# Performance work log

Measured on AMD Instinct MI355X. Metric: run time of the kernel, lower is better.

The kernel has to match this reference:

```python
import jax, jax.numpy as jnp
import numpy as np

S, LC = 4096, 16
N_WORD, N_CHAR = 100000, 128
CHAR_DIM, CHAR_HIDDEN = 64, 128
N_DIM, N_HIDDEN, N_TAG = 256, 512, 64


def setup_inputs() -> dict:
    key = jax.random.key(0)
    ks = jax.random.split(key, 16)
    rn = lambda k, shape, s=0.1: (jax.random.normal(k, shape, jnp.float32) * s)
    inp = {
        'char_emb': rn(ks[0], (N_CHAR, CHAR_DIM), 1.0),
        'char_Wih': rn(ks[1], (4 * CHAR_HIDDEN, CHAR_DIM)),
        'char_Whh': rn(ks[2], (4 * CHAR_HIDDEN, CHAR_HIDDEN)),
        'char_bih': rn(ks[3], (4 * CHAR_HIDDEN,)),
        'char_bhh': rn(ks[4], (4 * CHAR_HIDDEN,)),
        'word_emb': rn(ks[5], (N_WORD, N_DIM), 1.0),
        'Wih': rn(ks[6], (4 * N_HIDDEN, N_DIM + CHAR_HIDDEN)),
        'Whh': rn(ks[7], (4 * N_HIDDEN, N_HIDDEN)),
        'bih': rn(ks[8], (4 * N_HIDDEN,)),
        'bhh': rn(ks[9], (4 * N_HIDDEN,)),
        'W1': rn(ks[10], (N_TAG, N_HIDDEN)),
        'b1': rn(ks[11], (N_TAG,)),
        'x': jax.random.randint(ks[12], (S,), 0, N_WORD),
        'chars': jax.random.randint(ks[13], (S, LC), 0, N_CHAR),
        'char_lens': jax.random.randint(ks[14], (S,), 1, LC + 1),
    }
    return inp


def _lstm(xs, mask, Wih, Whh, bih, bhh):
    # xs: [T, B, In], mask: [T, B] bool. PyTorch gate order: i, f, g, o.
    T, B, _ = xs.shape
    H = Whh.shape[1]
    def step(carry, inp):
        h, c = carry
        x_t, m_t = inp
        g = x_t @ Wih.T + bih + h @ Whh.T + bhh  # [B, 4H]
        i, f, gg, o = jnp.split(g, 4, axis=-1)
        c_new = jax.nn.sigmoid(f) * c + jax.nn.sigmoid(i) * jnp.tanh(gg)
        h_new = jax.nn.sigmoid(o) * jnp.tanh(c_new)
        m = m_t[:, None]
        h2 = jnp.where(m, h_new, h)
        c2 = jnp.where(m, c_new, c)
        return (h2, c2), h2
    init = (jnp.zeros((B, H), xs.dtype), jnp.zeros((B, H), xs.dtype))
    (h_fin, _), hs = jax.lax.scan(step, init, (xs, mask))
    return hs, h_fin


def reference(char_emb, char_Wih, char_Whh, char_bih, char_bhh,
              word_emb, Wih, Whh, bih, bhh, W1, b1,
              x, chars, char_lens):
    # --- char-level LSTM, all S words batched (replaces per-word Python loop) ---
    cx = char_emb[chars]                      # [S, LC, char_dim]
    cx = jnp.transpose(cx, (1, 0, 2))         # [LC, S, char_dim]
    cmask = jnp.arange(LC)[:, None] < char_lens[None, :]  # [LC, S]
    _, char_h = _lstm(cx, cmask, char_Wih, char_Whh, char_bih, char_bhh)  # [S, char_hidden]

    # --- word-level LSTM over the sentence (batch 1, as in original) ---
    wx = word_emb[x]                          # [S, n_dim]
    feat = jnp.concatenate([wx, char_h], axis=-1)[:, None, :]  # [S, 1, n_dim+char_hidden]
    wmask = jnp.ones((feat.shape[0], 1), bool)
    hs, _ = _lstm(feat, wmask, Wih, Whh, bih, bhh)  # [S, 1, n_hidden]
    hs = hs[:, 0, :]

    logits = hs @ W1.T + b1                   # [S, n_tag]
    return jax.nn.log_softmax(logits, axis=-1)
```

## Files before the change

### kernel.cpp

```cpp
#include <hip/hip_runtime.h>
#include <hip/hip_bf16.h>


#define OFF_FLAG  0
#define OFF_CEMB  16
#define OFF_CWIH  8208
#define OFF_CBIH  40976
#define OFF_CBHH  41488
#define OFF_CWHH  42000
#define OFF_BIH   107536
#define OFF_BHH   109584
#define OFF_W1T   111632
#define OFF_CGE   144400
#define OFF_CH    209936
#define OFF_XP2   734224
#define OFF_HH    4928528

#define SENT 0xFFFFFFFFu

__device__ __forceinline__ float sigf(float x) { return 1.0f / (1.0f + __expf(-x)); }
__device__ __forceinline__ float tanh_f(float x) { return 2.0f * sigf(2.0f * x) - 1.0f; }
__device__ __forceinline__ float b2f_lo(unsigned u) { return __uint_as_float(u << 16); }
__device__ __forceinline__ float b2f_hi(unsigned u) { return __uint_as_float(u & 0xFFFF0000u); }
__device__ __forceinline__ float4 dec2(uint2 u) {
    return make_float4(b2f_lo(u.x), b2f_hi(u.x), b2f_lo(u.y), b2f_hi(u.y));
}

__global__ void detect_kernel(const unsigned* __restrict__ w, int* __restrict__ flagp) {
    unsigned v = w[threadIdx.x];
    unsigned e = (v >> 7) & 0xFF;
    int inr = (e >= 100 && e <= 140) ? 1 : 0;
    unsigned long long m = __ballot(inr);
    if (threadIdx.x == 0) flagp[0] = (__popcll(m) >= 56) ? 1 : 0;
}

__global__ void convf_kernel(const void* __restrict__ s, float* __restrict__ d,
                             int n, const int* __restrict__ flagp) {
    int i = blockIdx.x * 256 + threadIdx.x;
    if (i >= n) return;
    d[i] = flagp[0] ? __bfloat162float(((const __hip_bfloat16*)s)[i])
                    : ((const float*)s)[i];
}

__global__ void w1t_kernel(const void* __restrict__ W1, float* __restrict__ W1T,
                           const int* __restrict__ flagp) {
    int i = blockIdx.x * 256 + threadIdx.x;
    int j = i & 63, k = i >> 6;
    W1T[i] = flagp[0] ? __bfloat162float(((const __hip_bfloat16*)W1)[j * 512 + k])
                      : ((const float*)W1)[j * 512 + k];
}

__global__ void __launch_bounds__(256) cge_kernel(
    const float* __restrict__ cemb, const float* __restrict__ cWih,
    const float* __restrict__ cbih, const float* __restrict__ cbhh,
    float* __restrict__ cge)
{
    __shared__ float xe[64];
    int c = blockIdx.x, tid = threadIdx.x;
    if (tid < 64) xe[tid] = cemb[c * 64 + tid];
    __syncthreads();
#pragma unroll
    for (int rep = 0; rep < 2; ++rep) {
        int j = rep * 256 + tid;
        float acc = cbih[j] + cbhh[j];
#pragma unroll 8
        for (int k = 0; k < 64; ++k)
            acc += xe[k] * cWih[j * 64 + k];
        cge[c * 512 + j] = acc;
    }
}

__global__ void __launch_bounds__(256) char_lstm_kernel(
    const float* __restrict__ cge, const float* __restrict__ Whh,
    const int* __restrict__ chars, const int* __restrict__ lens,
    float* __restrict__ char_h)
{
    __shared__ float hls[16][128];
    int tid = threadIdx.x;
    int wl = tid >> 4, sl = tid & 15;
    int w = blockIdx.x * 16 + wl;
    int len = lens[w];
    const int* cw = chars + w * 16;
    float c[8];
#pragma unroll
    for (int q = 0; q < 8; ++q) { c[q] = 0.0f; hls[wl][sl * 8 + q] = 0.0f; }

    for (int t = 0; t < 16; ++t) {
        __syncthreads();
        int ch = cw[t];
        const float* xg = cge + ch * 512;
        float acc[4][8];
#pragma unroll
        for (int g = 0; g < 4; ++g)
#pragma unroll
            for (int q = 0; q < 8; ++q)
                acc[g][q] = xg[g * 128 + sl * 8 + q];

        const float4* h4 = (const float4*)hls[wl];
#pragma unroll
        for (int g = 0; g < 4; ++g) {
            const float4* wbase = ((const float4*)Whh) + (g * 128 + sl * 8) * 32;
            for (int k4 = 0; k4 < 32; ++k4) {
                float4 hv = h4[k4];
#pragma unroll
                for (int q = 0; q < 8; ++q) {
                    float4 wv = wbase[q * 32 + k4];
                    acc[g][q] += wv.x * hv.x + wv.y * hv.y + wv.z * hv.z + wv.w * hv.w;
                }
            }
        }
        __syncthreads();
        if (t < len) {
#pragma unroll
            for (int q = 0; q < 8; ++q) {
                float iv = sigf(acc[0][q]);
                float fv = sigf(acc[1][q]);
                float gv = tanh_f(acc[2][q]);
                float ov = sigf(acc[3][q]);
                c[q] = fv * c[q] + iv * gv;
                hls[wl][sl * 8 + q] = ov * tanh_f(c[q]);
            }
        }
    }
    __syncthreads();
#pragma unroll
    for (int q = 0; q < 8; ++q)
        char_h[w * 128 + sl * 8 + q] = hls[wl][sl * 8 + q];
}

__global__ void __launch_bounds__(256) xp2_kernel(
    const void* __restrict__ wemb, const int* __restrict__ x,
    const float* __restrict__ char_h, const void* __restrict__ Wraw,
    const float* __restrict__ bih, const float* __restrict__ bhh,
    __hip_bfloat16* __restrict__ xp2, const int* __restrict__ flagp)
{
    __shared__ float feat[16][384];
    int flag = flagp[0];
    int tid = threadIdx.x, tl = tid >> 4, sl = tid & 15;
    int t = blockIdx.x * 16 + tl;
    int xw = x[t];
    for (int idx = sl; idx < 384; idx += 16) {
        float v;
        if (idx < 256)
            v = flag ? __bfloat162float(((const __hip_bfloat16*)wemb)[(size_t)xw * 256 + idx])
                     : ((const float*)wemb)[(size_t)xw * 256 + idx];
        else
            v = char_h[t * 128 + (idx - 256)];
        feat[tl][idx] = v;
    }
    __syncthreads();

    const float4* f4 = (const float4*)feat[tl];
    for (int rb = 0; rb < 4; ++rb) {
        int r0 = rb * 512 + sl * 32;
        for (int qc = 0; qc < 4; ++qc) {
            int rr = r0 + qc * 8;
            float acc[8];
#pragma unroll
            for (int q = 0; q < 8; ++q)
                acc[q] = bih[rr + q] + bhh[rr + q];
            if (!flag) {
                const float4* wb = ((const float4*)Wraw) + (size_t)rr * 96;
                for (int k4 = 0; k4 < 96; ++k4) {
                    float4 fv = f4[k4];
#pragma unroll
                    for (int q = 0; q < 8; ++q) {
                        float4 wv = wb[q * 96 + k4];
                        acc[q] += wv.x * fv.x + wv.y * fv.y + wv.z * fv.z + wv.w * fv.w;
                    }
                }
            } else {
                const uint2* wb = ((const uint2*)Wraw) + (size_t)rr * 96;
                for (int k4 = 0; k4 < 96; ++k4) {
                    float4 fv = f4[k4];
#pragma unroll
                    for (int q = 0; q < 8; ++q) {
                        uint2 wv = wb[q * 96 + k4];
                        acc[q] += b2f_lo(wv.x) * fv.x + b2f_hi(wv.x) * fv.y
                                + b2f_lo(wv.y) * fv.z + b2f_hi(wv.y) * fv.w;
                    }
                }
            }
#pragma unroll
            for (int q = 0; q < 8; ++q)
                xp2[(size_t)t * 2048 + rr + q] = __float2bfloat16(acc[q]);
        }
    }
}

__global__ void __launch_bounds__(256, 1) word_lstm_kernel(
    const __hip_bfloat16* __restrict__ xp2, const void* __restrict__ Whh_raw,
    float* __restrict__ h_hist, const int* __restrict__ flagp)
{
    __shared__ float hbuf[4][576];
    int flag = flagp[0];
    int tid = threadIdx.x;
    int wave = tid >> 6, lane = tid & 63;
    int wgid = blockIdx.x * 4 + wave;
    int sp = lane >> 5;
    int g  = (lane >> 3) & 3;
    int kk = lane & 7;
    int slot = wgid * 2 + sp;
    int grow = g * 512 + slot;

    float4 w00, w01, w02, w03, w04, w05, w06, w07;
    float4 w08, w09, w10, w11, w12, w13, w14, w15;
    if (!flag) {
        const float4* wr = (const float4*)((const float*)Whh_raw + (size_t)grow * 512 + kk * 64);
        w00 = wr[0];  w01 = wr[1];  w02 = wr[2];  w03 = wr[3];
        w04 = wr[4];  w05 = wr[5];  w06 = wr[6];  w07 = wr[7];
        w08 = wr[8];  w09 = wr[9];  w10 = wr[10]; w11 = wr[11];
        w12 = wr[12]; w13 = wr[13]; w14 = wr[14]; w15 = wr[15];
    } else {
        const uint2* wr = (const uint2*)((const unsigned short*)Whh_raw + (size_t)grow * 512 + kk * 64);
        w00 = dec2(wr[0]);  w01 = dec2(wr[1]);  w02 = dec2(wr[2]);  w03 = dec2(wr[3]);
        w04 = dec2(wr[4]);  w05 = dec2(wr[5]);  w06 = dec2(wr[6]);  w07 = dec2(wr[7]);
        w08 = dec2(wr[8]);  w09 = dec2(wr[9]);  w10 = dec2(wr[10]); w11 = dec2(wr[11]);
        w12 = dec2(wr[12]); w13 = dec2(wr[13]); w14 = dec2(wr[14]); w15 = dec2(wr[15]);
    }

    unsigned* hview = (unsigned*)h_hist;
    const unsigned short* xpr = (const unsigned short*)xp2;
    float* wbuf = hbuf[wave];
    float c = 0.0f;
    int dead = 0;

    unsigned short xraw = xpr[grow];

    for (int t = 0; t < 4096; ++t) {
        unsigned short xraw_nx = (t < 4095) ? xpr[(size_t)(t + 1) * 2048 + grow] : (unsigned short)0;

        if (t == 0) {
#pragma unroll
            for (int i = 0; i < 8; ++i)
                wbuf[(2 * i + (lane >> 5)) * 36 + (lane & 31)] = 0.0f;
        } else {
            const unsigned* src = hview + (size_t)(t - 1) * 512 + lane;
            unsigned v[8];
            unsigned spins = 0;
            for (;;) {
#pragma unroll
                for (int i = 0; i < 8; ++i)
                    v[i] = __hip_atomic_load(src + (size_t)i * 64, __ATOMIC_RELAXED,
                                             __HIP_MEMORY_SCOPE_AGENT);
                int ok = 1;
#pragma unroll
                for (int i = 0; i < 8; ++i) ok &= (v[i] != SENT);
                if (dead || __all(ok)) break;
                if (++spins > (1u << 22)) { dead = 1; break; }
            }
            if (dead) {
#pragma unroll
                for (int i = 0; i < 8; ++i)
                    if (v[i] == SENT) v[i] = __float_as_uint(12345.0f);
            }
#pragma unroll
            for (int i = 0; i < 8; ++i)
                wbuf[(2 * i + (lane >> 5)) * 36 + (lane & 31)] = __uint_as_float(v[i]);
        }

        const float4* p0 = (const float4*)(wbuf + kk * 72);
        const float4* p1 = (const float4*)(wbuf + kk * 72 + 36);
        float a0 = 0.0f, a1 = 0.0f, a2 = 0.0f, a3 = 0.0f;
        {
            float4 hv;
#define FMA4_(A, W, HV) A += (W).x*(HV).x + (W).y*(HV).y + (W).z*(HV).z + (W).w*(HV).w
            hv = p0[0]; FMA4_(a0, w00, hv);  hv = p0[1]; FMA4_(a1, w01, hv);
            hv = p0[2]; FMA4_(a2, w02, hv);  hv = p0[3]; FMA4_(a3, w03, hv);
            hv = p0[4]; FMA4_(a0, w04, hv);  hv = p0[5]; FMA4_(a1, w05, hv);
            hv = p0[6]; FMA4_(a2, w06, hv);  hv = p0[7]; FMA4_(a3, w07, hv);
            hv = p1[0]; FMA4_(a0, w08, hv);  hv = p1[1]; FMA4_(a1, w09, hv);
            hv = p1[2]; FMA4_(a2, w10, hv);  hv = p1[3]; FMA4_(a3, w11, hv);
            hv = p1[4]; FMA4_(a0, w12, hv);  hv = p1[5]; FMA4_(a1, w13, hv);
            hv = p1[6]; FMA4_(a2, w14, hv);  hv = p1[7]; FMA4_(a3, w15, hv);
#undef FMA4_
        }
        float acc = (a0 + a1) + (a2 + a3);
        acc += __shfl_xor(acc, 1);
        acc += __shfl_xor(acc, 2);
        acc += __shfl_xor(acc, 4);
        float gvt = acc + __bfloat162float(*(const __hip_bfloat16*)&xraw);

        float iv = __shfl(gvt, sp * 32 + 0);
        float fv = __shfl(gvt, sp * 32 + 8);
        float gg = __shfl(gvt, sp * 32 + 16);
        float ov = __shfl(gvt, sp * 32 + 24);
        c = sigf(fv) * c + sigf(iv) * tanh_f(gg);
        float h = sigf(ov) * tanh_f(c);

        if ((lane & 31) == 0)
            __hip_atomic_store(hview + (size_t)t * 512 + slot,
                               __float_as_uint(h),
                               __ATOMIC_RELAXED, __HIP_MEMORY_SCOPE_AGENT);

        xraw = xraw_nx;
    }
}

__global__ void __launch_bounds__(64) out_kernel(
    const float* __restrict__ h_hist, const float* __restrict__ W1T,
    const void* __restrict__ b1raw, void* __restrict__ out,
    const int* __restrict__ flagp)
{
    __shared__ float hb[512];
    int flag = flagp[0];
    int t = blockIdx.x, j = threadIdx.x;
    const float4* src = (const float4*)(h_hist + (size_t)t * 512);
    ((float4*)hb)[j * 2] = src[j * 2];
    ((float4*)hb)[j * 2 + 1] = src[j * 2 + 1];
    __syncthreads();

    float acc = flag ? __bfloat162float(((const __hip_bfloat16*)b1raw)[j])
                     : ((const float*)b1raw)[j];
#pragma unroll 8
    for (int k = 0; k < 512; ++k)
        acc += hb[k] * W1T[k * 64 + j];

    float m = acc;
#pragma unroll
    for (int o = 32; o; o >>= 1) m = fmaxf(m, __shfl_xor(m, o));
    float e = __expf(acc - m);
    float s = e;
#pragma unroll
    for (int o = 32; o; o >>= 1) s += __shfl_xor(s, o);
    float r = acc - m - __logf(s);
    if (flag) ((__hip_bfloat16*)out)[t * 64 + j] = __float2bfloat16(r);
    else      ((float*)out)[t * 64 + j] = r;
}

extern "C" void kernel_launch(void* const* d_in, const int* in_sizes, int n_in,
                              void* d_out, int out_size, void* d_ws, size_t ws_size,
                              hipStream_t stream)
{
    (void)in_sizes; (void)n_in; (void)out_size; (void)ws_size;
    const void* char_emb = d_in[0];
    const void* char_Wih = d_in[1];
    const void* char_Whh = d_in[2];
    const void* char_bih = d_in[3];
    const void* char_bhh = d_in[4];
    const void* word_emb = d_in[5];
    const void* Wih      = d_in[6];
    const void* Whh      = d_in[7];
    const void* bih      = d_in[8];
    const void* bhh      = d_in[9];
    const void* W1       = d_in[10];
    const void* b1       = d_in[11];
    const int* x     = (const int*)d_in[12];
    const int* chars = (const int*)d_in[13];
    const int* lens  = (const int*)d_in[14];

    float* ws    = (float*)d_ws;
    int*   flagp = (int*)(ws + OFF_FLAG);
    float* cembf = ws + OFF_CEMB;
    float* cWihf = ws + OFF_CWIH;
    float* cbihf = ws + OFF_CBIH;
    float* cbhhf = ws + OFF_CBHH;
    float* cWhhf = ws + OFF_CWHH;
    float* bihf  = ws + OFF_BIH;
    float* bhhf  = ws + OFF_BHH;
    float* W1T   = ws + OFF_W1T;
    float* cge   = ws + OFF_CGE;
    float* charh = ws + OFF_CH;
    __hip_bfloat16* xp2 = (__hip_bfloat16*)(ws + OFF_XP2);
    float* hh    = ws + OFF_HH;

    hipMemsetAsync(hh, 0xFF, (size_t)4096 * 512 * 4, stream);

    detect_kernel<<<1, 64, 0, stream>>>((const unsigned*)char_emb, flagp);

    convf_kernel<<<(8192 + 255) / 256, 256, 0, stream>>>(char_emb, cembf, 8192, flagp);
    convf_kernel<<<(32768 + 255) / 256, 256, 0, stream>>>(char_Wih, cWihf, 32768, flagp);
    convf_kernel<<<2, 256, 0, stream>>>(char_bih, cbihf, 512, flagp);
    convf_kernel<<<2, 256, 0, stream>>>(char_bhh, cbhhf, 512, flagp);
    convf_kernel<<<(65536 + 255) / 256, 256, 0, stream>>>(char_Whh, cWhhf, 65536, flagp);
    convf_kernel<<<8, 256, 0, stream>>>(bih, bihf, 2048, flagp);
    convf_kernel<<<8, 256, 0, stream>>>(bhh, bhhf, 2048, flagp);
    w1t_kernel<<<128, 256, 0, stream>>>(W1, W1T, flagp);

    cge_kernel<<<128, 256, 0, stream>>>(cembf, cWihf, cbihf, cbhhf, cge);
    char_lstm_kernel<<<256, 256, 0, stream>>>(cge, cWhhf, chars, lens, charh);
    xp2_kernel<<<256, 256, 0, stream>>>(word_emb, x, charh, Wih, bihf, bhhf, xp2, flagp);
    word_lstm_kernel<<<64, 256, 0, stream>>>(xp2, Whh, hh, flagp);
    out_kernel<<<4096, 64, 0, stream>>>(hh, W1T, b1, d_out, flagp);
}
```

Baseline: 14.65 ms.

## Pack word-LSTM hidden exchange into bf16 pairs with 16 large workgroups

The word-level LSTM moves from 64 blocks of 256 threads to 16 blocks of 1024 threads. Each block gathers its 32 hidden outputs in shared memory behind a barrier and publishes them as packed bf16 pairs with one store per lane. Each block reads its own slice from shared memory at full precision and polls only the other blocks' words. This halves the bytes moved through global memory per step and cuts the number of polling producers, at the cost of a __syncthreads per step and bf16 rounding of the exchanged hidden state. The output kernel is updated to read bf16 hidden history.

```diff
diff --git a/kernel.cpp b/kernel.cpp
--- a/kernel.cpp
+++ b/kernel.cpp
@@ -25,6 +25,11 @@
 __device__ __forceinline__ float4 dec2(uint2 u) {
     return make_float4(b2f_lo(u.x), b2f_hi(u.x), b2f_lo(u.y), b2f_hi(u.y));
 }
+__device__ __forceinline__ unsigned f2bf_bits(float f) {
+    unsigned b = __float_as_uint(f);
+    b += 0x7FFFu + ((b >> 16) & 1u);
+    return b >> 16;
+}
 
 __global__ void detect_kernel(const unsigned* __restrict__ w, int* __restrict__ flagp) {
     unsigned v = w[threadIdx.x];
@@ -188,20 +193,22 @@
     }
 }
 
-__global__ void __launch_bounds__(256, 1) word_lstm_kernel(
+__global__ void __launch_bounds__(1024, 4) word_lstm_kernel(
     const __hip_bfloat16* __restrict__ xp2, const void* __restrict__ Whh_raw,
-    float* __restrict__ h_hist, const int* __restrict__ flagp)
-{
-    __shared__ float hbuf[4][576];
+    unsigned* __restrict__ hview, const int* __restrict__ flagp)
+{
+    __shared__ float hbuf[16][576];
+    __shared__ float hout[2][32];
     int flag = flagp[0];
+    int wg = blockIdx.x;
     int tid = threadIdx.x;
     int wave = tid >> 6, lane = tid & 63;
-    int wgid = blockIdx.x * 4 + wave;
     int sp = lane >> 5;
     int g  = (lane >> 3) & 3;
     int kk = lane & 7;
-    int slot = wgid * 2 + sp;
+    int slot = wg * 32 + wave * 2 + sp;
     int grow = g * 512 + slot;
+    int ownidx = ((lane >> 4) == (wg & 3)) ? (wg >> 2) : -1;
 
     float4 w00, w01, w02, w03, w04, w05, w06, w07;
     float4 w08, w09, w10, w11, w12, w13, w14, w15;
@@ -218,45 +225,60 @@
         w08 = dec2(wr[8]);  w09 = dec2(wr[9]);  w10 = dec2(wr[10]); w11 = dec2(wr[11]);
         w12 = dec2(wr[12]); w13 = dec2(wr[13]); w14 = dec2(wr[14]); w15 = dec2(wr[15]);
     }
-
-    unsigned* hview = (unsigned*)h_hist;
+#define PIN4(a,b,c,d) asm volatile("" : "+v"(a.x),"+v"(a.y),"+v"(a.z),"+v"(a.w), \
+    "+v"(b.x),"+v"(b.y),"+v"(b.z),"+v"(b.w), "+v"(c.x),"+v"(c.y),"+v"(c.z),"+v"(c.w), \
+    "+v"(d.x),"+v"(d.y),"+v"(d.z),"+v"(d.w))
+    PIN4(w00, w01, w02, w03); PIN4(w04, w05, w06, w07);
+    PIN4(w08, w09, w10, w11); PIN4(w12, w13, w14, w15);
+#undef PIN4
+
     const unsigned short* xpr = (const unsigned short*)xp2;
     float* wbuf = hbuf[wave];
     float c = 0.0f;
     int dead = 0;
 
-    unsigned short xraw = xpr[grow];
-
     for (int t = 0; t < 4096; ++t) {
-        unsigned short xraw_nx = (t < 4095) ? xpr[(size_t)(t + 1) * 2048 + grow] : (unsigned short)0;
+        unsigned short xraw = xpr[(size_t)t * 2048 + grow];
 
         if (t == 0) {
 #pragma unroll
             for (int i = 0; i < 8; ++i)
                 wbuf[(2 * i + (lane >> 5)) * 36 + (lane & 31)] = 0.0f;
         } else {
-            const unsigned* src = hview + (size_t)(t - 1) * 512 + lane;
-            unsigned v[8];
+            const unsigned* src = hview + (size_t)(t - 1) * 256;
+            const float* houtprev = hout[(t - 1) & 1];
+            unsigned v[4];
             unsigned spins = 0;
             for (;;) {
 #pragma unroll
-                for (int i = 0; i < 8; ++i)
-                    v[i] = __hip_atomic_load(src + (size_t)i * 64, __ATOMIC_RELAXED,
+                for (int i = 0; i < 4; ++i)
+                    v[i] = __hip_atomic_load(src + lane + i * 64, __ATOMIC_RELAXED,
                                              __HIP_MEMORY_SCOPE_AGENT);
                 int ok = 1;
 #pragma unroll
-                for (int i = 0; i < 8; ++i) ok &= (v[i] != SENT);
+                for (int i = 0; i < 4; ++i) ok &= (i == ownidx) | (v[i] != SENT);
                 if (dead || __all(ok)) break;
                 if (++spins > (1u << 22)) { dead = 1; break; }
             }
             if (dead) {
 #pragma unroll
-                for (int i = 0; i < 8; ++i)
-                    if (v[i] == SENT) v[i] = __float_as_uint(12345.0f);
-            }
-#pragma unroll
-            for (int i = 0; i < 8; ++i)
-                wbuf[(2 * i + (lane >> 5)) * 36 + (lane & 31)] = __uint_as_float(v[i]);
+                for (int i = 0; i < 4; ++i)
+                    if (i != ownidx && v[i] == SENT) v[i] = 0x3f803f80u;
+            }
+#pragma unroll
+            for (int i = 0; i < 4; ++i) {
+                int ch = (lane >> 4) + 4 * i;
+                float f0, f1;
+                if (i == ownidx) {
+                    f0 = houtprev[2 * (lane & 15)];
+                    f1 = houtprev[2 * (lane & 15) + 1];
+                } else {
+                    f0 = b2f_lo(v[i]);
+                    f1 = b2f_hi(v[i]);
+                }
+                wbuf[ch * 36 + 2 * (lane & 15)]     = f0;
+                wbuf[ch * 36 + 2 * (lane & 15) + 1] = f1;
+            }
         }
 
         const float4* p0 = (const float4*)(wbuf + kk * 72);
@@ -288,26 +310,34 @@
         c = sigf(fv) * c + sigf(iv) * tanh_f(gg);
         float h = sigf(ov) * tanh_f(c);
 
-        if ((lane & 31) == 0)
-            __hip_atomic_store(hview + (size_t)t * 512 + slot,
-                               __float_as_uint(h),
+        if ((lane & 31) == 0) hout[t & 1][wave * 2 + sp] = h;
+        __syncthreads();
+
+        if (wave == 0 && lane < 16) {
+            unsigned u0 = f2bf_bits(hout[t & 1][2 * lane]);
+            unsigned u1 = f2bf_bits(hout[t & 1][2 * lane + 1]);
+            __hip_atomic_store(hview + (size_t)t * 256 + wg * 16 + lane,
+                               u0 | (u1 << 16),
                                __ATOMIC_RELAXED, __HIP_MEMORY_SCOPE_AGENT);
-
-        xraw = xraw_nx;
+        }
     }
 }
 
 __global__ void __launch_bounds__(64) out_kernel(
-    const float* __restrict__ h_hist, const float* __restrict__ W1T,
+    const unsigned short* __restrict__ hh16, const float* __restrict__ W1T,
     const void* __restrict__ b1raw, void* __restrict__ out,
     const int* __restrict__ flagp)
 {
     __shared__ float hb[512];
     int flag = flagp[0];
     int t = blockIdx.x, j = threadIdx.x;
-    const float4* src = (const float4*)(h_hist + (size_t)t * 512);
-    ((float4*)hb)[j * 2] = src[j * 2];
-    ((float4*)hb)[j * 2 + 1] = src[j * 2 + 1];
+    const unsigned* src = (const unsigned*)(hh16 + (size_t)t * 512);
+#pragma unroll
+    for (int kq = 0; kq < 4; ++kq) {
+        unsigned u = src[j * 4 + kq];
+        hb[j * 8 + 2 * kq]     = b2f_lo(u);
+        hb[j * 8 + 2 * kq + 1] = b2f_hi(u);
+    }
     __syncthreads();
 
     float acc = flag ? __bfloat162float(((const __hip_bfloat16*)b1raw)[j])
@@ -362,9 +392,9 @@
     float* cge   = ws + OFF_CGE;
     float* charh = ws + OFF_CH;
     __hip_bfloat16* xp2 = (__hip_bfloat16*)(ws + OFF_XP2);
-    float* hh    = ws + OFF_HH;
-
-    hipMemsetAsync(hh, 0xFF, (size_t)4096 * 512 * 4, stream);
+    unsigned short* hh16 = (unsigned short*)(ws + OFF_HH);
+
+    hipMemsetAsync(hh16, 0xFF, (size_t)4096 * 512 * 2, stream);
 
     detect_kernel<<<1, 64, 0, stream>>>((const unsigned*)char_emb, flagp);
 
@@ -380,6 +410,6 @@
     cge_kernel<<<128, 256, 0, stream>>>(cembf, cWihf, cbihf, cbhhf, cge);
     char_lstm_kernel<<<256, 256, 0, stream>>>(cge, cWhhf, chars, lens, charh);
     xp2_kernel<<<256, 256, 0, stream>>>(word_emb, x, charh, Wih, bihf, bhhf, xp2, flagp);
-    word_lstm_kernel<<<64, 256, 0, stream>>>(xp2, Whh, hh, flagp);
-    out_kernel<<<4096, 64, 0, stream>>>(hh, W1T, b1, d_out, flagp);
-}
+    word_lstm_kernel<<<16, 1024, 0, stream>>>(xp2, Whh, (unsigned*)hh16, flagp);
+    out_kernel<<<4096, 64, 0, stream>>>(hh16, W1T, b1, d_out, flagp);
+}
```

Measured after the change: 13.85 ms. 5.5% less time.
